# Optimization experiments

Hardware: AMD Instinct MI355X
Metric: run time of the kernel (lower is better)

## Reference

```python
import jax, jax.numpy as jnp
import numpy as np

B, N, H, D, E = 32, 1000, 256, 128, 512000
NB = B * N


def setup_inputs() -> dict:
    key = jax.random.key(0)
    ks = jax.random.split(key, 16)
    s = 0.05
    inp = {
        "x": jax.random.normal(ks[0], (B, D), jnp.float32),
        "h_prev": jax.random.normal(ks[1], (B, N, H), jnp.float32),
        "c_prev": jax.random.normal(ks[2], (B, N, H), jnp.float32),
        "src": jax.random.randint(ks[3], (E,), 0, NB, jnp.int32),
        "dst": jax.random.randint(ks[4], (E,), 0, NB, jnp.int32),
        "Wi": jax.random.normal(ks[5], (D, H), jnp.float32) * s,
        "bi": jax.random.normal(ks[6], (H,), jnp.float32) * s,
        "Wf": jax.random.normal(ks[7], (D, H), jnp.float32) * s,
        "bf": jax.random.normal(ks[8], (H,), jnp.float32) * s,
        "Wo": jax.random.normal(ks[9], (D, H), jnp.float32) * s,
        "bo": jax.random.normal(ks[10], (H,), jnp.float32) * s,
        "Wc": jax.random.normal(ks[11], (D, H), jnp.float32) * s,
        "bc": jax.random.normal(ks[12], (H,), jnp.float32) * s,
        "Wg": jax.random.normal(ks[13], (H, H), jnp.float32) * s,
        "bg": jax.random.normal(ks[14], (H,), jnp.float32) * s,
    }
    return inp


def _graph_conv(src, dst, h, Wg, bg):
    # DGL GraphConv, norm='both': D_dst^{-1/2} * sum_edges (D_src^{-1/2} * h_src) @ W + b
    nb = h.shape[0]
    ones = jnp.ones(src.shape[0], h.dtype)
    deg_out = jnp.maximum(jax.ops.segment_sum(ones, src, num_segments=nb), 1.0)
    deg_in = jnp.maximum(jax.ops.segment_sum(ones, dst, num_segments=nb), 1.0)
    h = h * (deg_out ** -0.5)[:, None]          # pre-normalize by src out-degree
    agg = jax.ops.segment_sum(h[src], dst, num_segments=nb)  # irregular gather/scatter
    agg = agg * (deg_in ** -0.5)[:, None]       # post-normalize by dst in-degree
    return agg @ Wg + bg


def reference(x, h_prev, c_prev, src, dst, Wi, bi, Wf, bf, Wo, bo, Wc, bc, Wg, bg):
    b, n, hh = h_prev.shape
    h_conv = _graph_conv(src, dst, h_prev.reshape(b * n, hh), Wg, bg).reshape(b, n, hh)
    # four input-gate projections, broadcast over nodes
    xi = (x @ Wi + bi)[:, None, :]
    xf = (x @ Wf + bf)[:, None, :]
    xo = (x @ Wo + bo)[:, None, :]
    xc = (x @ Wc + bc)[:, None, :]
    i_t = jax.nn.sigmoid(xi + h_conv)
    f_t = jax.nn.sigmoid(xf + h_conv)
    o_t = jax.nn.sigmoid(xo + h_conv)
    c_tilde = jnp.tanh(xc + h_conv)
    c_t = f_t * c_prev + i_t * c_tilde
    h_t = o_t * jnp.tanh(c_t)
    return h_t, c_t
```

## Files before the change

kernel.cpp:

```cpp
#include <hip/hip_runtime.h>

#define BB 32
#define NN 1000
#define HH 256
#define DD 128
#define EE 512000
#define NB (BB * NN)
#define PADLOG 6
#define PAD (1 << PADLOG)

#define DEGO_OFF 0
#define DEGI_OFF (NB)
#define GATE_OFF (2 * NB)
#define WGB_OFF (GATE_OFF + 4 * BB * HH)
#define PADC_OFF (WGB_OFF + (HH * HH) / 2)
#define HW_OFF (PADC_OFF + NB * PAD)

using bf16x8 = __attribute__((ext_vector_type(8))) short;
using f32x4 = __attribute__((ext_vector_type(4))) float;

__device__ inline unsigned short f2bf(float x) {
    unsigned u = __float_as_uint(x);
    return (unsigned short)((u + 0x7FFFu + ((u >> 16) & 1u)) >> 16);
}
__device__ inline float bf2f(unsigned short u) {
    return __uint_as_float(((unsigned)u) << 16);
}

__global__ __launch_bounds__(256) void k_pre(
    int* __restrict__ deg_out, int* __restrict__ deg_in,
    const float* __restrict__ Wg, unsigned short* __restrict__ wgb,
    const float* __restrict__ x, const float* __restrict__ Wi,
    const float* __restrict__ bi, const float* __restrict__ Wf,
    const float* __restrict__ bf_, const float* __restrict__ Wo,
    const float* __restrict__ bo, const float* __restrict__ Wc,
    const float* __restrict__ bc, float* __restrict__ gates) {
    int blk = blockIdx.x;
    int t = threadIdx.x;
    if (blk < BB) {
        __shared__ float xs[DD];
        int b = blk;
        if (t < DD) xs[t] = x[b * DD + t];
        __syncthreads();
        float ai = bi[t], af = bf_[t], ao = bo[t], ac = bc[t];
#pragma unroll 4
        for (int k = 0; k < DD; k++) {
            float xv = xs[k];
            ai += xv * Wi[k * HH + t];
            af += xv * Wf[k * HH + t];
            ao += xv * Wo[k * HH + t];
            ac += xv * Wc[k * HH + t];
        }
        gates[0 * BB * HH + b * HH + t] = ai;
        gates[1 * BB * HH + b * HH + t] = af;
        gates[2 * BB * HH + b * HH + t] = ao;
        gates[3 * BB * HH + b * HH + t] = ac;
    } else if (blk < BB + 256) {
        int o = (blk - BB) * 256 + t;
        int j = o & 7;
        int c = o >> 3;
        int lane = c & 63;
        int nt = (c >> 6) & 15;
        int kk = c >> 10;
        int k = kk * 32 + (lane >> 4) * 8 + j;
        int n = nt * 16 + (lane & 15);
        wgb[o] = f2bf(Wg[k * HH + n]);
    } else {
        int idx = (blk - (BB + 256)) * 256 + t;
        deg_out[idx] = 0;
        deg_in[idx] = 0;
    }
}

__global__ __launch_bounds__(256) void k_mid(
    const int* __restrict__ src, const int* __restrict__ dst,
    int* __restrict__ deg_out, int* __restrict__ deg_in,
    int* __restrict__ padded, const float* __restrict__ h,
    const unsigned short* __restrict__ wgb, unsigned short* __restrict__ hw) {
    int blk = blockIdx.x;
    if (blk < NB / 64) {
        int t = threadIdx.x;
        int lane = t & 63;
        int w = t >> 6;
        int quad = lane >> 4;
        int mrow = lane & 15;
        int r0 = blk * 64 + w * 16;
        int row = r0 + mrow;

        f32x4 acc[16];
#pragma unroll
        for (int nt = 0; nt < 16; nt++) acc[nt] = (f32x4){0.f, 0.f, 0.f, 0.f};

#pragma unroll 1
        for (int kk = 0; kk < 8; kk++) {
            const float* ap = h + (size_t)row * HH + kk * 32 + quad * 8;
            float4 a0 = *(const float4*)ap;
            float4 a1 = *(const float4*)(ap + 4);
            bf16x8 af;
            af[0] = (short)f2bf(a0.x);
            af[1] = (short)f2bf(a0.y);
            af[2] = (short)f2bf(a0.z);
            af[3] = (short)f2bf(a0.w);
            af[4] = (short)f2bf(a1.x);
            af[5] = (short)f2bf(a1.y);
            af[6] = (short)f2bf(a1.z);
            af[7] = (short)f2bf(a1.w);
#pragma unroll
            for (int nt = 0; nt < 16; nt++) {
                bf16x8 bfr =
                    *(const bf16x8*)(wgb + (((kk * 16 + nt) * 64 + lane) << 3));
                acc[nt] = __builtin_amdgcn_mfma_f32_16x16x32_bf16(af, bfr,
                                                                  acc[nt], 0,
                                                                  0, 0);
            }
        }
#pragma unroll
        for (int nt = 0; nt < 16; nt++) {
#pragma unroll
            for (int reg = 0; reg < 4; reg++) {
                hw[(size_t)(r0 + quad * 4 + reg) * HH + nt * 16 + mrow] =
                    f2bf(acc[nt][reg]);
            }
        }
    } else {
        int e = (blk - NB / 64) * 256 + threadIdx.x;
        int s = src[e];
        int d = dst[e];
        atomicAdd(&deg_out[s], 1);
        int p = atomicAdd(&deg_in[d], 1);
        if (p < PAD) padded[(d << PADLOG) + p] = s;
    }
}

__device__ inline void lstm1(float hc, float gi, float gf, float go, float gc,
                             float cp, float& ho, float& co) {
    float pi = gi + hc, pf = gf + hc, po = go + hc, pc = gc + hc;
    float it = 1.f / (1.f + __expf(-pi));
    float ft = 1.f / (1.f + __expf(-pf));
    float ot = 1.f / (1.f + __expf(-po));
    float e2 = __expf(2.f * pc);
    float ctl = (e2 - 1.f) / (e2 + 1.f);
    float ct = ft * cp + it * ctl;
    float e2c = __expf(2.f * ct);
    ho = ot * (e2c - 1.f) / (e2c + 1.f);
    co = ct;
}

__global__ __launch_bounds__(256) void k_out(
    const unsigned short* __restrict__ hw, const int* __restrict__ padded,
    const int* __restrict__ deg_in, const int* __restrict__ deg_out,
    const float* __restrict__ bg, const float* __restrict__ gates,
    const float* __restrict__ c_prev, float* __restrict__ h_out,
    float* __restrict__ c_out) {
    int t = threadIdx.x;
    int lane = t & 63;
    int w = t >> 6;
    int node = blockIdx.x * 4 + w;
    int dcnt = deg_in[node];
    float si = rsqrtf((float)max(dcnt, 1));
    int cnt = min(dcnt, PAD);
    int beg = node << PADLOG;
    int end = beg + cnt;
    int col = lane * 4;
    const unsigned short* hwc = hw + col;

    float ax = 0.f, ay = 0.f, az = 0.f, aw = 0.f;
    int e = beg;
    for (; e + 8 <= end; e += 8) {
        int s0 = padded[e + 0];
        int s1 = padded[e + 1];
        int s2 = padded[e + 2];
        int s3 = padded[e + 3];
        int s4 = padded[e + 4];
        int s5 = padded[e + 5];
        int s6 = padded[e + 6];
        int s7 = padded[e + 7];
        float c0 = rsqrtf((float)max(deg_out[s0], 1));
        float c1 = rsqrtf((float)max(deg_out[s1], 1));
        float c2 = rsqrtf((float)max(deg_out[s2], 1));
        float c3 = rsqrtf((float)max(deg_out[s3], 1));
        float c4 = rsqrtf((float)max(deg_out[s4], 1));
        float c5 = rsqrtf((float)max(deg_out[s5], 1));
        float c6 = rsqrtf((float)max(deg_out[s6], 1));
        float c7 = rsqrtf((float)max(deg_out[s7], 1));
        ushort4 q0 = *(const ushort4*)(hwc + ((size_t)s0 << 8));
        ushort4 q1 = *(const ushort4*)(hwc + ((size_t)s1 << 8));
        ushort4 q2 = *(const ushort4*)(hwc + ((size_t)s2 << 8));
        ushort4 q3 = *(const ushort4*)(hwc + ((size_t)s3 << 8));
        ushort4 q4 = *(const ushort4*)(hwc + ((size_t)s4 << 8));
        ushort4 q5 = *(const ushort4*)(hwc + ((size_t)s5 << 8));
        ushort4 q6 = *(const ushort4*)(hwc + ((size_t)s6 << 8));
        ushort4 q7 = *(const ushort4*)(hwc + ((size_t)s7 << 8));
        ax += ((c0 * bf2f(q0.x) + c1 * bf2f(q1.x)) +
               (c2 * bf2f(q2.x) + c3 * bf2f(q3.x))) +
              ((c4 * bf2f(q4.x) + c5 * bf2f(q5.x)) +
               (c6 * bf2f(q6.x) + c7 * bf2f(q7.x)));
        ay += ((c0 * bf2f(q0.y) + c1 * bf2f(q1.y)) +
               (c2 * bf2f(q2.y) + c3 * bf2f(q3.y))) +
              ((c4 * bf2f(q4.y) + c5 * bf2f(q5.y)) +
               (c6 * bf2f(q6.y) + c7 * bf2f(q7.y)));
        az += ((c0 * bf2f(q0.z) + c1 * bf2f(q1.z)) +
               (c2 * bf2f(q2.z) + c3 * bf2f(q3.z))) +
              ((c4 * bf2f(q4.z) + c5 * bf2f(q5.z)) +
               (c6 * bf2f(q6.z) + c7 * bf2f(q7.z)));
        aw += ((c0 * bf2f(q0.w) + c1 * bf2f(q1.w)) +
               (c2 * bf2f(q2.w) + c3 * bf2f(q3.w))) +
              ((c4 * bf2f(q4.w) + c5 * bf2f(q5.w)) +
               (c6 * bf2f(q6.w) + c7 * bf2f(q7.w)));
    }
    for (; e < end; e++) {
        int s = padded[e];
        float cc = rsqrtf((float)max(deg_out[s], 1));
        ushort4 q = *(const ushort4*)(hwc + ((size_t)s << 8));
        ax += cc * bf2f(q.x);
        ay += cc * bf2f(q.y);
        az += cc * bf2f(q.z);
        aw += cc * bf2f(q.w);
    }

    int b = node / NN;
    float4 bgv = *(const float4*)(bg + col);
    float4 gi = *(const float4*)(gates + 0 * BB * HH + b * HH + col);
    float4 gf = *(const float4*)(gates + 1 * BB * HH + b * HH + col);
    float4 go = *(const float4*)(gates + 2 * BB * HH + b * HH + col);
    float4 gc = *(const float4*)(gates + 3 * BB * HH + b * HH + col);
    float4 cp = *(const float4*)(c_prev + (size_t)node * HH + col);

    float4 ho, co;
    lstm1(ax * si + bgv.x, gi.x, gf.x, go.x, gc.x, cp.x, ho.x, co.x);
    lstm1(ay * si + bgv.y, gi.y, gf.y, go.y, gc.y, cp.y, ho.y, co.y);
    lstm1(az * si + bgv.z, gi.z, gf.z, go.z, gc.z, cp.z, ho.z, co.z);
    lstm1(aw * si + bgv.w, gi.w, gf.w, go.w, gc.w, cp.w, ho.w, co.w);

    *(float4*)(h_out + (size_t)node * HH + col) = ho;
    *(float4*)(c_out + (size_t)node * HH + col) = co;
}

extern "C" void kernel_launch(void* const* d_in, const int* in_sizes, int n_in,
                              void* d_out, int out_size, void* d_ws,
                              size_t ws_size, hipStream_t stream) {
    const float* x = (const float*)d_in[0];
    const float* h_prev = (const float*)d_in[1];
    const float* c_prev = (const float*)d_in[2];
    const int* src = (const int*)d_in[3];
    const int* dst = (const int*)d_in[4];
    const float* Wi = (const float*)d_in[5];
    const float* bi = (const float*)d_in[6];
    const float* Wf = (const float*)d_in[7];
    const float* bf_ = (const float*)d_in[8];
    const float* Wo = (const float*)d_in[9];
    const float* bo = (const float*)d_in[10];
    const float* Wc = (const float*)d_in[11];
    const float* bc = (const float*)d_in[12];
    const float* Wg = (const float*)d_in[13];
    const float* bg = (const float*)d_in[14];

    int* wsi = (int*)d_ws;
    float* wsf = (float*)d_ws;
    int* deg_out = wsi + DEGO_OFF;
    int* deg_in = wsi + DEGI_OFF;
    float* gates = wsf + GATE_OFF;
    unsigned short* wgb = (unsigned short*)(wsi + WGB_OFF);
    int* padded = wsi + PADC_OFF;
    unsigned short* hw = (unsigned short*)(wsi + HW_OFF);
    float* h_out = (float*)d_out;
    float* c_out = h_out + (size_t)NB * HH;

    k_pre<<<BB + 256 + NB / 256, 256, 0, stream>>>(
        deg_out, deg_in, Wg, wgb, x, Wi, bi, Wf, bf_, Wo, bo, Wc, bc, gates);
    k_mid<<<NB / 64 + EE / 256, 256, 0, stream>>>(src, dst, deg_out, deg_in,
                                                  padded, h_prev, wgb, hw);
    k_out<<<NB / 4, 256, 0, stream>>>(hw, padded, deg_in, deg_out, bg, gates,
                                      c_prev, h_out, c_out);
}
```

Measured before the change: 257.1 us.

## Split degree counters into four sub-buckets and pack neighbor lists as 16-bit indices

```diff
diff --git a/kernel.cpp b/kernel.cpp
--- a/kernel.cpp
+++ b/kernel.cpp
@@ -6,15 +6,15 @@
 #define DD 128
 #define EE 512000
 #define NB (BB * NN)
-#define PADLOG 6
-#define PAD (1 << PADLOG)
+#define PSUB 24
+#define PTOT 96
 
 #define DEGO_OFF 0
-#define DEGI_OFF (NB)
-#define GATE_OFF (2 * NB)
+#define CUR_OFF (4 * NB)
+#define GATE_OFF (8 * NB)
 #define WGB_OFF (GATE_OFF + 4 * BB * HH)
-#define PADC_OFF (WGB_OFF + (HH * HH) / 2)
-#define HW_OFF (PADC_OFF + NB * PAD)
+#define PAD_OFF (WGB_OFF + (HH * HH) / 2)
+#define HW_OFF (PAD_OFF + NB * PTOT / 2)
 
 using bf16x8 = __attribute__((ext_vector_type(8))) short;
 using f32x4 = __attribute__((ext_vector_type(4))) float;
@@ -28,7 +28,6 @@
 }
 
 __global__ __launch_bounds__(256) void k_pre(
-    int* __restrict__ deg_out, int* __restrict__ deg_in,
     const float* __restrict__ Wg, unsigned short* __restrict__ wgb,
     const float* __restrict__ x, const float* __restrict__ Wi,
     const float* __restrict__ bi, const float* __restrict__ Wf,
@@ -55,7 +54,7 @@
         gates[1 * BB * HH + b * HH + t] = af;
         gates[2 * BB * HH + b * HH + t] = ao;
         gates[3 * BB * HH + b * HH + t] = ac;
-    } else if (blk < BB + 256) {
+    } else {
         int o = (blk - BB) * 256 + t;
         int j = o & 7;
         int c = o >> 3;
@@ -65,17 +64,13 @@
         int k = kk * 32 + (lane >> 4) * 8 + j;
         int n = nt * 16 + (lane & 15);
         wgb[o] = f2bf(Wg[k * HH + n]);
-    } else {
-        int idx = (blk - (BB + 256)) * 256 + t;
-        deg_out[idx] = 0;
-        deg_in[idx] = 0;
     }
 }
 
 __global__ __launch_bounds__(256) void k_mid(
     const int* __restrict__ src, const int* __restrict__ dst,
-    int* __restrict__ deg_out, int* __restrict__ deg_in,
-    int* __restrict__ padded, const float* __restrict__ h,
+    int* __restrict__ dego4, int* __restrict__ cur,
+    unsigned short* __restrict__ pad16, const float* __restrict__ h,
     const unsigned short* __restrict__ wgb, unsigned short* __restrict__ hw) {
     int blk = blockIdx.x;
     if (blk < NB / 64) {
@@ -123,12 +118,18 @@
             }
         }
     } else {
-        int e = (blk - NB / 64) * 256 + threadIdx.x;
-        int s = src[e];
-        int d = dst[e];
-        atomicAdd(&deg_out[s], 1);
-        int p = atomicAdd(&deg_in[d], 1);
-        if (p < PAD) padded[(d << PADLOG) + p] = s;
+        int i = (blk - NB / 64) * 256 + threadIdx.x;
+        int2 sv = *(const int2*)(src + 2 * i);
+        int2 dv = *(const int2*)(dst + 2 * i);
+        int e0 = 2 * i;
+        int ra = e0 & 3;
+        int rb = ra + 1;
+        atomicAdd(&dego4[sv.x * 4 + ra], 1);
+        atomicAdd(&dego4[sv.y * 4 + rb], 1);
+        int p0 = atomicAdd(&cur[ra * NB + dv.x], 1);
+        int p1 = atomicAdd(&cur[rb * NB + dv.y], 1);
+        if (p0 < PSUB) pad16[dv.x * PTOT + p0 * 4 + ra] = (unsigned short)sv.x;
+        if (p1 < PSUB) pad16[dv.y * PTOT + p1 * 4 + rb] = (unsigned short)sv.y;
     }
 }
 
@@ -147,75 +148,72 @@
 }
 
 __global__ __launch_bounds__(256) void k_out(
-    const unsigned short* __restrict__ hw, const int* __restrict__ padded,
-    const int* __restrict__ deg_in, const int* __restrict__ deg_out,
-    const float* __restrict__ bg, const float* __restrict__ gates,
-    const float* __restrict__ c_prev, float* __restrict__ h_out,
-    float* __restrict__ c_out) {
+    const unsigned short* __restrict__ hw,
+    const unsigned short* __restrict__ pad16, const int* __restrict__ cur,
+    const int* __restrict__ dego4, const float* __restrict__ bg,
+    const float* __restrict__ gates, const float* __restrict__ c_prev,
+    float* __restrict__ h_out, float* __restrict__ c_out) {
     int t = threadIdx.x;
     int lane = t & 63;
     int w = t >> 6;
     int node = blockIdx.x * 4 + w;
-    int dcnt = deg_in[node];
-    float si = rsqrtf((float)max(dcnt, 1));
-    int cnt = min(dcnt, PAD);
-    int beg = node << PADLOG;
-    int end = beg + cnt;
+    int c0 = cur[0 * NB + node];
+    int c1 = cur[1 * NB + node];
+    int c2 = cur[2 * NB + node];
+    int c3 = cur[3 * NB + node];
+    int tot = c0 + c1 + c2 + c3;
+    float si = rsqrtf((float)max(tot, 1));
+    c0 = min(c0, PSUB);
+    c1 = min(c1, PSUB);
+    c2 = min(c2, PSUB);
+    c3 = min(c3, PSUB);
+    int m4 = 4 * min(min(c0, c1), min(c2, c3));
+    int M4 = 4 * max(max(c0, c1), max(c2, c3));
+    unsigned pk = (unsigned)c0 | ((unsigned)c1 << 8) | ((unsigned)c2 << 16) |
+                  ((unsigned)c3 << 24);
+    const unsigned short* pl = pad16 + node * PTOT;
     int col = lane * 4;
     const unsigned short* hwc = hw + col;
 
     float ax = 0.f, ay = 0.f, az = 0.f, aw = 0.f;
-    int e = beg;
-    for (; e + 8 <= end; e += 8) {
-        int s0 = padded[e + 0];
-        int s1 = padded[e + 1];
-        int s2 = padded[e + 2];
-        int s3 = padded[e + 3];
-        int s4 = padded[e + 4];
-        int s5 = padded[e + 5];
-        int s6 = padded[e + 6];
-        int s7 = padded[e + 7];
-        float c0 = rsqrtf((float)max(deg_out[s0], 1));
-        float c1 = rsqrtf((float)max(deg_out[s1], 1));
-        float c2 = rsqrtf((float)max(deg_out[s2], 1));
-        float c3 = rsqrtf((float)max(deg_out[s3], 1));
-        float c4 = rsqrtf((float)max(deg_out[s4], 1));
-        float c5 = rsqrtf((float)max(deg_out[s5], 1));
-        float c6 = rsqrtf((float)max(deg_out[s6], 1));
-        float c7 = rsqrtf((float)max(deg_out[s7], 1));
+    int j = 0;
+    for (; j < m4; j += 4) {
+        ushort4 ss = *(const ushort4*)(pl + j);
+        int s0 = ss.x, s1 = ss.y, s2 = ss.z, s3 = ss.w;
+        int4 g0 = *(const int4*)(dego4 + s0 * 4);
+        int4 g1 = *(const int4*)(dego4 + s1 * 4);
+        int4 g2 = *(const int4*)(dego4 + s2 * 4);
+        int4 g3 = *(const int4*)(dego4 + s3 * 4);
+        float cc0 = rsqrtf((float)max(g0.x + g0.y + g0.z + g0.w, 1));
+        float cc1 = rsqrtf((float)max(g1.x + g1.y + g1.z + g1.w, 1));
+        float cc2 = rsqrtf((float)max(g2.x + g2.y + g2.z + g2.w, 1));
+        float cc3 = rsqrtf((float)max(g3.x + g3.y + g3.z + g3.w, 1));
         ushort4 q0 = *(const ushort4*)(hwc + ((size_t)s0 << 8));
         ushort4 q1 = *(const ushort4*)(hwc + ((size_t)s1 << 8));
         ushort4 q2 = *(const ushort4*)(hwc + ((size_t)s2 << 8));
         ushort4 q3 = *(const ushort4*)(hwc + ((size_t)s3 << 8));
-        ushort4 q4 = *(const ushort4*)(hwc + ((size_t)s4 << 8));
-        ushort4 q5 = *(const ushort4*)(hwc + ((size_t)s5 << 8));
-        ushort4 q6 = *(const ushort4*)(hwc + ((size_t)s6 << 8));
-        ushort4 q7 = *(const ushort4*)(hwc + ((size_t)s7 << 8));
-        ax += ((c0 * bf2f(q0.x) + c1 * bf2f(q1.x)) +
-               (c2 * bf2f(q2.x) + c3 * bf2f(q3.x))) +
-              ((c4 * bf2f(q4.x) + c5 * bf2f(q5.x)) +
-               (c6 * bf2f(q6.x) + c7 * bf2f(q7.x)));
-        ay += ((c0 * bf2f(q0.y) + c1 * bf2f(q1.y)) +
-               (c2 * bf2f(q2.y) + c3 * bf2f(q3.y))) +
-              ((c4 * bf2f(q4.y) + c5 * bf2f(q5.y)) +
-               (c6 * bf2f(q6.y) + c7 * bf2f(q7.y)));
-        az += ((c0 * bf2f(q0.z) + c1 * bf2f(q1.z)) +
-               (c2 * bf2f(q2.z) + c3 * bf2f(q3.z))) +
-              ((c4 * bf2f(q4.z) + c5 * bf2f(q5.z)) +
-               (c6 * bf2f(q6.z) + c7 * bf2f(q7.z)));
-        aw += ((c0 * bf2f(q0.w) + c1 * bf2f(q1.w)) +
-               (c2 * bf2f(q2.w) + c3 * bf2f(q3.w))) +
-              ((c4 * bf2f(q4.w) + c5 * bf2f(q5.w)) +
-               (c6 * bf2f(q6.w) + c7 * bf2f(q7.w)));
-    }
-    for (; e < end; e++) {
-        int s = padded[e];
-        float cc = rsqrtf((float)max(deg_out[s], 1));
-        ushort4 q = *(const ushort4*)(hwc + ((size_t)s << 8));
-        ax += cc * bf2f(q.x);
-        ay += cc * bf2f(q.y);
-        az += cc * bf2f(q.z);
-        aw += cc * bf2f(q.w);
+        ax += (cc0 * bf2f(q0.x) + cc1 * bf2f(q1.x)) +
+              (cc2 * bf2f(q2.x) + cc3 * bf2f(q3.x));
+        ay += (cc0 * bf2f(q0.y) + cc1 * bf2f(q1.y)) +
+              (cc2 * bf2f(q2.y) + cc3 * bf2f(q3.y));
+        az += (cc0 * bf2f(q0.z) + cc1 * bf2f(q1.z)) +
+              (cc2 * bf2f(q2.z) + cc3 * bf2f(q3.z));
+        aw += (cc0 * bf2f(q0.w) + cc1 * bf2f(q1.w)) +
+              (cc2 * bf2f(q2.w) + cc3 * bf2f(q3.w));
+    }
+    for (; j < M4; j++) {
+        int r = j & 3;
+        int p = j >> 2;
+        if (((pk >> (r * 8)) & 255u) > (unsigned)p) {
+            int s = pl[j];
+            int4 g = *(const int4*)(dego4 + s * 4);
+            float cc = rsqrtf((float)max(g.x + g.y + g.z + g.w, 1));
+            ushort4 q = *(const ushort4*)(hwc + ((size_t)s << 8));
+            ax += cc * bf2f(q.x);
+            ay += cc * bf2f(q.y);
+            az += cc * bf2f(q.z);
+            aw += cc * bf2f(q.w);
+        }
     }
 
     int b = node / NN;
@@ -257,19 +255,21 @@
 
     int* wsi = (int*)d_ws;
     float* wsf = (float*)d_ws;
-    int* deg_out = wsi + DEGO_OFF;
-    int* deg_in = wsi + DEGI_OFF;
+    int* dego4 = wsi + DEGO_OFF;
+    int* cur = wsi + CUR_OFF;
     float* gates = wsf + GATE_OFF;
     unsigned short* wgb = (unsigned short*)(wsi + WGB_OFF);
-    int* padded = wsi + PADC_OFF;
+    unsigned short* pad16 = (unsigned short*)(wsi + PAD_OFF);
     unsigned short* hw = (unsigned short*)(wsi + HW_OFF);
     float* h_out = (float*)d_out;
     float* c_out = h_out + (size_t)NB * HH;
 
-    k_pre<<<BB + 256 + NB / 256, 256, 0, stream>>>(
-        deg_out, deg_in, Wg, wgb, x, Wi, bi, Wf, bf_, Wo, bo, Wc, bc, gates);
-    k_mid<<<NB / 64 + EE / 256, 256, 0, stream>>>(src, dst, deg_out, deg_in,
-                                                  padded, h_prev, wgb, hw);
-    k_out<<<NB / 4, 256, 0, stream>>>(hw, padded, deg_in, deg_out, bg, gates,
+    hipMemsetAsync(dego4, 0, (size_t)8 * NB * 4, stream);
+
+    k_pre<<<BB + 256, 256, 0, stream>>>(Wg, wgb, x, Wi, bi, Wf, bf_, Wo, bo,
+                                        Wc, bc, gates);
+    k_mid<<<NB / 64 + EE / 512, 256, 0, stream>>>(src, dst, dego4, cur, pad16,
+                                                  h_prev, wgb, hw);
+    k_out<<<NB / 4, 256, 0, stream>>>(hw, pad16, cur, dego4, bg, gates,
                                       c_prev, h_out, c_out);
 }
```

Measured after the change: 280.3 us. 1.09x slower.

## Replace global atomic edge scatter with two-pass bucketed binning in LDS

Applied to the files above, without the earlier changes.

```diff
diff --git a/kernel.cpp b/kernel.cpp
--- a/kernel.cpp
+++ b/kernel.cpp
@@ -6,15 +6,22 @@
 #define DD 128
 #define EE 512000
 #define NB (BB * NN)
-#define PADLOG 6
-#define PAD (1 << PADLOG)
-
-#define DEGO_OFF 0
-#define DEGI_OFF (NB)
-#define GATE_OFF (2 * NB)
+#define NBKT 250
+#define BKTCAP 2560
+#define EPB 2000
+#define NP1 256
+#define PADS 64
+
+#define GCURD_OFF 0
+#define GCURS_OFF (NBKT)
+#define DEGI_OFF 512
+#define DEGO_OFF (512 + NB)
+#define GATE_OFF (512 + 2 * NB)
 #define WGB_OFF (GATE_OFF + 4 * BB * HH)
-#define PADC_OFF (WGB_OFF + (HH * HH) / 2)
-#define HW_OFF (PADC_OFF + NB * PAD)
+#define DSTB_OFF (WGB_OFF + (HH * HH) / 2)
+#define SRCB_OFF (DSTB_OFF + NBKT * BKTCAP)
+#define PAD_OFF (SRCB_OFF + NBKT * BKTCAP / 2)
+#define HW_OFF (PAD_OFF + NB * PADS / 2)
 
 using bf16x8 = __attribute__((ext_vector_type(8))) short;
 using f32x4 = __attribute__((ext_vector_type(4))) float;
@@ -28,7 +35,9 @@
 }
 
 __global__ __launch_bounds__(256) void k_pre(
-    int* __restrict__ deg_out, int* __restrict__ deg_in,
+    const int* __restrict__ src, const int* __restrict__ dst,
+    int* __restrict__ gcurD, int* __restrict__ gcurS,
+    unsigned* __restrict__ dstb, unsigned short* __restrict__ srcb,
     const float* __restrict__ Wg, unsigned short* __restrict__ wgb,
     const float* __restrict__ x, const float* __restrict__ Wi,
     const float* __restrict__ bi, const float* __restrict__ Wf,
@@ -66,20 +75,47 @@
         int n = nt * 16 + (lane & 15);
         wgb[o] = f2bf(Wg[k * HH + n]);
     } else {
-        int idx = (blk - (BB + 256)) * 256 + t;
-        deg_out[idx] = 0;
-        deg_in[idx] = 0;
+        __shared__ int cntD[NBKT], cntS[NBKT], posD[NBKT], posS[NBKT];
+        int pb = blk - (BB + 256);
+        int e0 = pb * EPB;
+        for (int i = t; i < NBKT; i += 256) {
+            cntD[i] = 0;
+            cntS[i] = 0;
+        }
+        __syncthreads();
+        for (int i = t; i < EPB; i += 256) {
+            int s = src[e0 + i];
+            int d = dst[e0 + i];
+            atomicAdd(&cntS[s >> 7], 1);
+            atomicAdd(&cntD[d >> 7], 1);
+        }
+        __syncthreads();
+        for (int i = t; i < NBKT; i += 256) {
+            posD[i] = atomicAdd(&gcurD[i], cntD[i]);
+            posS[i] = atomicAdd(&gcurS[i], cntS[i]);
+        }
+        __syncthreads();
+        for (int i = t; i < EPB; i += 256) {
+            int s = src[e0 + i];
+            int d = dst[e0 + i];
+            int bd = d >> 7, bs = s >> 7;
+            int pd = atomicAdd(&posD[bd], 1);
+            int ps = atomicAdd(&posS[bs], 1);
+            dstb[bd * BKTCAP + pd] = ((unsigned)s << 16) | (unsigned)d;
+            srcb[bs * BKTCAP + ps] = (unsigned short)s;
+        }
     }
 }
 
 __global__ __launch_bounds__(256) void k_mid(
-    const int* __restrict__ src, const int* __restrict__ dst,
-    int* __restrict__ deg_out, int* __restrict__ deg_in,
-    int* __restrict__ padded, const float* __restrict__ h,
+    const int* __restrict__ gcurD, const int* __restrict__ gcurS,
+    const unsigned* __restrict__ dstb, const unsigned short* __restrict__ srcb,
+    unsigned short* __restrict__ pad16, int* __restrict__ deg_in,
+    int* __restrict__ deg_out, const float* __restrict__ h,
     const unsigned short* __restrict__ wgb, unsigned short* __restrict__ hw) {
     int blk = blockIdx.x;
+    int t = threadIdx.x;
     if (blk < NB / 64) {
-        int t = threadIdx.x;
         int lane = t & 63;
         int w = t >> 6;
         int quad = lane >> 4;
@@ -122,13 +158,36 @@
                     f2bf(acc[nt][reg]);
             }
         }
+    } else if (blk < NB / 64 + NBKT) {
+        __shared__ unsigned short lpad[128 * PADS];
+        __shared__ int lcnt[128];
+        int qb = blk - NB / 64;
+        if (t < 128) lcnt[t] = 0;
+        __syncthreads();
+        int n = gcurD[qb];
+        const unsigned* eb = dstb + qb * BKTCAP;
+        for (int i = t; i < n; i += 256) {
+            unsigned p = eb[i];
+            int s = (int)(p >> 16);
+            int dl = (int)(p & 127u);
+            int q = atomicAdd(&lcnt[dl], 1);
+            if (q < PADS) lpad[dl * PADS + q] = (unsigned short)s;
+        }
+        __syncthreads();
+        int* gp = (int*)(pad16 + (size_t)qb * 128 * PADS);
+        const int* lp = (const int*)lpad;
+        for (int i = t; i < 128 * PADS / 2; i += 256) gp[i] = lp[i];
+        if (t < 128) deg_in[qb * 128 + t] = lcnt[t];
     } else {
-        int e = (blk - NB / 64) * 256 + threadIdx.x;
-        int s = src[e];
-        int d = dst[e];
-        atomicAdd(&deg_out[s], 1);
-        int p = atomicAdd(&deg_in[d], 1);
-        if (p < PAD) padded[(d << PADLOG) + p] = s;
+        __shared__ int scnt[128];
+        int qb = blk - (NB / 64 + NBKT);
+        if (t < 128) scnt[t] = 0;
+        __syncthreads();
+        int n = gcurS[qb];
+        const unsigned short* sb = srcb + qb * BKTCAP;
+        for (int i = t; i < n; i += 256) atomicAdd(&scnt[sb[i] & 127], 1);
+        __syncthreads();
+        if (t < 128) deg_out[qb * 128 + t] = scnt[t];
     }
 }
 
@@ -147,34 +206,29 @@
 }
 
 __global__ __launch_bounds__(256) void k_out(
-    const unsigned short* __restrict__ hw, const int* __restrict__ padded,
-    const int* __restrict__ deg_in, const int* __restrict__ deg_out,
-    const float* __restrict__ bg, const float* __restrict__ gates,
-    const float* __restrict__ c_prev, float* __restrict__ h_out,
-    float* __restrict__ c_out) {
+    const unsigned short* __restrict__ hw,
+    const unsigned short* __restrict__ pad16, const int* __restrict__ deg_in,
+    const int* __restrict__ deg_out, const float* __restrict__ bg,
+    const float* __restrict__ gates, const float* __restrict__ c_prev,
+    float* __restrict__ h_out, float* __restrict__ c_out) {
     int t = threadIdx.x;
     int lane = t & 63;
     int w = t >> 6;
     int node = blockIdx.x * 4 + w;
     int dcnt = deg_in[node];
     float si = rsqrtf((float)max(dcnt, 1));
-    int cnt = min(dcnt, PAD);
-    int beg = node << PADLOG;
-    int end = beg + cnt;
+    int cnt = min(dcnt, PADS);
+    const unsigned short* pl = pad16 + (size_t)node * PADS;
     int col = lane * 4;
     const unsigned short* hwc = hw + col;
 
     float ax = 0.f, ay = 0.f, az = 0.f, aw = 0.f;
-    int e = beg;
-    for (; e + 8 <= end; e += 8) {
-        int s0 = padded[e + 0];
-        int s1 = padded[e + 1];
-        int s2 = padded[e + 2];
-        int s3 = padded[e + 3];
-        int s4 = padded[e + 4];
-        int s5 = padded[e + 5];
-        int s6 = padded[e + 6];
-        int s7 = padded[e + 7];
+    int e = 0;
+    for (; e + 8 <= cnt; e += 8) {
+        ushort4 sa = *(const ushort4*)(pl + e);
+        ushort4 sb = *(const ushort4*)(pl + e + 4);
+        int s0 = sa.x, s1 = sa.y, s2 = sa.z, s3 = sa.w;
+        int s4 = sb.x, s5 = sb.y, s6 = sb.z, s7 = sb.w;
         float c0 = rsqrtf((float)max(deg_out[s0], 1));
         float c1 = rsqrtf((float)max(deg_out[s1], 1));
         float c2 = rsqrtf((float)max(deg_out[s2], 1));
@@ -208,8 +262,8 @@
               ((c4 * bf2f(q4.w) + c5 * bf2f(q5.w)) +
                (c6 * bf2f(q6.w) + c7 * bf2f(q7.w)));
     }
-    for (; e < end; e++) {
-        int s = padded[e];
+    for (; e < cnt; e++) {
+        int s = pl[e];
         float cc = rsqrtf((float)max(deg_out[s], 1));
         ushort4 q = *(const ushort4*)(hwc + ((size_t)s << 8));
         ax += cc * bf2f(q.x);
@@ -257,19 +311,27 @@
 
     int* wsi = (int*)d_ws;
     float* wsf = (float*)d_ws;
+    int* gcurD = wsi + GCURD_OFF;
+    int* gcurS = wsi + GCURS_OFF;
+    int* deg_in = wsi + DEGI_OFF;
     int* deg_out = wsi + DEGO_OFF;
-    int* deg_in = wsi + DEGI_OFF;
     float* gates = wsf + GATE_OFF;
     unsigned short* wgb = (unsigned short*)(wsi + WGB_OFF);
-    int* padded = wsi + PADC_OFF;
+    unsigned* dstb = (unsigned*)(wsi + DSTB_OFF);
+    unsigned short* srcb = (unsigned short*)(wsi + SRCB_OFF);
+    unsigned short* pad16 = (unsigned short*)(wsi + PAD_OFF);
     unsigned short* hw = (unsigned short*)(wsi + HW_OFF);
     float* h_out = (float*)d_out;
     float* c_out = h_out + (size_t)NB * HH;
 
-    k_pre<<<BB + 256 + NB / 256, 256, 0, stream>>>(
-        deg_out, deg_in, Wg, wgb, x, Wi, bi, Wf, bf_, Wo, bo, Wc, bc, gates);
-    k_mid<<<NB / 64 + EE / 256, 256, 0, stream>>>(src, dst, deg_out, deg_in,
-                                                  padded, h_prev, wgb, hw);
-    k_out<<<NB / 4, 256, 0, stream>>>(hw, padded, deg_in, deg_out, bg, gates,
+    hipMemsetAsync(gcurD, 0, (size_t)2 * NBKT * 4, stream);
+
+    k_pre<<<BB + 256 + NP1, 256, 0, stream>>>(src, dst, gcurD, gcurS, dstb,
+                                              srcb, Wg, wgb, x, Wi, bi, Wf,
+                                              bf_, Wo, bo, Wc, bc, gates);
+    k_mid<<<NB / 64 + 2 * NBKT, 256, 0, stream>>>(gcurD, gcurS, dstb, srcb,
+                                                  pad16, deg_in, deg_out,
+                                                  h_prev, wgb, hw);
+    k_out<<<NB / 4, 256, 0, stream>>>(hw, pad16, deg_in, deg_out, bg, gates,
                                       c_prev, h_out, c_out);
 }
```

After: 238.1 us, median of 2. 7.4% less time.
